# Performance work log

Hardware: AMD Instinct MI355X
Metric: run time of the kernel (lower is better)

The kernel has to match this reference:

```python
import jax, jax.numpy as jnp
import numpy as np

Q_SIZE, K_SIZE, H = 256, 256, 128
N, n, m, D_V = 4, 512, 512, 256

def setup_inputs() -> dict:
    key = jax.random.key(0)
    k1, k2, k3, k4, k5, k6 = jax.random.split(key, 6)
    return {
        "query": jax.random.normal(k1, (N, n, Q_SIZE), dtype=jnp.float32),
        "key": jax.random.normal(k2, (N, m, K_SIZE), dtype=jnp.float32),
        "value": jax.random.normal(k3, (N, m, D_V), dtype=jnp.float32),
        "W_q": jax.random.normal(k4, (Q_SIZE, H), dtype=jnp.float32) / np.sqrt(Q_SIZE),
        "W_k": jax.random.normal(k5, (K_SIZE, H), dtype=jnp.float32) / np.sqrt(K_SIZE),
        "W_v": jax.random.normal(k6, (H,), dtype=jnp.float32) / np.sqrt(H),
    }

def reference(query, key, value, W_q, W_k, W_v):
    q = query @ W_q                      # (N, n, h)
    k = key @ W_k                        # (N, m, h)
    # broadcast additive scores: tanh((N,n,1,h) + (N,1,m,h)) reduced by W_v -> (N,n,m)
    feats = jnp.tanh(q[:, :, None, :] + k[:, None, :, :])
    scores = jnp.einsum('bnmh,h->bnm', feats, W_v)
    attn = jax.nn.softmax(scores, axis=-1)  # softmax over keys m
    return jnp.einsum('bnm,bmd->bnd', attn, value)
```

## Files before the change

### kernel.cpp

```cpp
#include <hip/hip_runtime.h>
#include <math.h>

#define NB   4
#define SEQN 512
#define SEQM 512
#define QS   256
#define HH   128
#define DV   256
#define BM   (NB * SEQM)

static constexpr float kPreScale = 2.8853900817779268f;
static constexpr float kLog2e    = 1.4426950408889634f;

#if __has_builtin(__builtin_amdgcn_exp2f)
__device__ __forceinline__ float fexp2(float x) { return __builtin_amdgcn_exp2f(x); }
#else
__device__ __forceinline__ float fexp2(float x) { return exp2f(x); }
#endif

#if __has_builtin(__builtin_amdgcn_rcpf)
__device__ __forceinline__ float frcp(float x) { return __builtin_amdgcn_rcpf(x); }
#else
__device__ __forceinline__ float frcp(float x) { return 1.0f / x; }
#endif

__global__ __launch_bounds__(512) void proj_kernel(
    const float* __restrict__ query, const float* __restrict__ key,
    const float* __restrict__ Wq, const float* __restrict__ Wk,
    const float* __restrict__ wv,
    float* __restrict__ qt, float2* __restrict__ kt) {
  const int t = threadIdx.x;
  const int half = (NB * SEQN) / 8;
  const bool isK = blockIdx.x >= half;
  const int rb   = isK ? (blockIdx.x - half) : blockIdx.x;
  const float* __restrict__ in = isK ? key : query;
  const float* __restrict__ W  = isK ? Wk  : Wq;
  const int row0 = rb * 8;

  const int j  = t & 127;
  const int r0 = __builtin_amdgcn_readfirstlane((t >> 7) * 2);

  const float* __restrict__ x0p = in + (size_t)(row0 + r0 + 0) * QS;
  const float* __restrict__ x1p = in + (size_t)(row0 + r0 + 1) * QS;

  float a0 = 0.f, a1 = 0.f;
  for (int k0 = 0; k0 < QS; k0 += 4) {
    const float w0 = W[(k0 + 0) * HH + j];
    const float w1 = W[(k0 + 1) * HH + j];
    const float w2 = W[(k0 + 2) * HH + j];
    const float w3 = W[(k0 + 3) * HH + j];
    const float4 x0 = *reinterpret_cast<const float4*>(x0p + k0);
    const float4 x1 = *reinterpret_cast<const float4*>(x1p + k0);
    a0 = fmaf(x0.x, w0, fmaf(x0.y, w1, fmaf(x0.z, w2, fmaf(x0.w, w3, a0))));
    a1 = fmaf(x1.x, w0, fmaf(x1.y, w1, fmaf(x1.z, w2, fmaf(x1.w, w3, a1))));
  }
  const float wvj = wv[j];
  float acc[2] = {a0, a1};
#pragma unroll
  for (int r = 0; r < 2; ++r) {
    const float e  = fexp2(acc[r] * kPreScale);
    const float rc = frcp(e + 1.0f);
    float A = fmaf(-2.0f, rc, 1.0f);
    A = fminf(fmaxf(A, -0.99999988f), 0.99999988f);
    const int grow = row0 + r0 + r;
    if (isK) {
      kt[(size_t)j * BM + grow] = make_float2(A, wvj * A);
    } else {
      qt[(size_t)grow * (2 * HH) + j]      = A;
      qt[(size_t)grow * (2 * HH) + HH + j] = wvj * A;
    }
  }
}

__global__ __launch_bounds__(1024) void fused_kernel(
    const float* __restrict__ qt, const float2* __restrict__ kt,
    const float* __restrict__ value, float* __restrict__ out) {
  __shared__ float sp[8][SEQM];
  __shared__ float pvbuf[4][8][DV];
  __shared__ float rsh[8];

  const int t  = threadIdx.x;
  const int b  = blockIdx.x >> 6;
  const int n0 = (blockIdx.x & 63) * 8;
  const int m  = t & 511;
  const int nq4 = __builtin_amdgcn_readfirstlane((t >> 9) * 4);

  const float* __restrict__ qb = qt + ((size_t)b * SEQN + n0 + nq4) * (2 * HH);
  const float2* __restrict__ kb = kt + (size_t)b * SEQM + m;

  float N[4], D[4];
#pragma unroll
  for (int n = 0; n < 4; ++n) { N[n] = 0.f; D[n] = 1.f; }

  float2 fb[8];
#pragma unroll
  for (int jj = 0; jj < 8; ++jj) fb[jj] = kb[(size_t)jj * BM];

  for (int h0 = 0; h0 < HH; h0 += 8) {
    float kA[8], kW[8];
#pragma unroll
    for (int jj = 0; jj < 8; ++jj) { kA[jj] = fb[jj].x; kW[jj] = fb[jj].y; }
    if (h0 + 8 < HH) {
#pragma unroll
      for (int jj = 0; jj < 8; ++jj) fb[jj] = kb[(size_t)(h0 + 8 + jj) * BM];
    }
#pragma unroll
    for (int n = 0; n < 4; ++n) {
      const float* qr = qb + n * (2 * HH);
      const float4 a0 = *reinterpret_cast<const float4*>(qr + h0);
      const float4 a1 = *reinterpret_cast<const float4*>(qr + h0 + 4);
      const float4 v0 = *reinterpret_cast<const float4*>(qr + HH + h0);
      const float4 v1 = *reinterpret_cast<const float4*>(qr + HH + h0 + 4);
      const float s0 = v0.x + kW[0], d0 = fmaf(a0.x, kA[0], 1.0f);
      const float s1 = v0.y + kW[1], d1 = fmaf(a0.y, kA[1], 1.0f);
      const float s2 = v0.z + kW[2], d2 = fmaf(a0.z, kA[2], 1.0f);
      const float s3 = v0.w + kW[3], d3 = fmaf(a0.w, kA[3], 1.0f);
      const float s4 = v1.x + kW[4], d4 = fmaf(a1.x, kA[4], 1.0f);
      const float s5 = v1.y + kW[5], d5 = fmaf(a1.y, kA[5], 1.0f);
      const float s6 = v1.z + kW[6], d6 = fmaf(a1.z, kA[6], 1.0f);
      const float s7 = v1.w + kW[7], d7 = fmaf(a1.w, kA[7], 1.0f);
      const float t01 = fmaf(s0, d1, s1 * d0), e01 = d0 * d1;
      const float t23 = fmaf(s2, d3, s3 * d2), e23 = d2 * d3;
      const float t45 = fmaf(s4, d5, s5 * d4), e45 = d4 * d5;
      const float t67 = fmaf(s6, d7, s7 * d6), e67 = d6 * d7;
      const float t03 = fmaf(t01, e23, t23 * e01), e03 = e01 * e23;
      const float t47 = fmaf(t45, e67, t67 * e45), e47 = e45 * e67;
      const float t07 = fmaf(t03, e47, t47 * e03), e07 = e03 * e47;
      N[n] = fmaf(N[n], e07, t07 * D[n]);
      D[n] *= e07;
    }
  }
#pragma unroll
  for (int n = 0; n < 4; ++n) sp[nq4 + n][m] = N[n] * frcp(D[n]);
  __syncthreads();

  const int wave = t >> 6;
  const int lane = t & 63;
  const int row  = wave >> 1;
  const int hf   = wave & 1;
  float v[8];
  float mx = -1e30f;
#pragma unroll
  for (int i = 0; i < 8; ++i) {
    v[i] = sp[row][lane + 64 * i];
    mx = fmaxf(mx, v[i]);
  }
#pragma unroll
  for (int off = 32; off > 0; off >>= 1) mx = fmaxf(mx, __shfl_xor(mx, off));
  float p[8];
  float sum = 0.f;
#pragma unroll
  for (int i = 0; i < 8; ++i) {
    p[i] = fexp2((v[i] - mx) * kLog2e);
    sum += p[i];
  }
#pragma unroll
  for (int off = 32; off > 0; off >>= 1) sum += __shfl_xor(sum, off);
  __syncthreads();
#pragma unroll
  for (int i = 4 * hf; i < 4 * hf + 4; ++i) sp[row][lane + 64 * i] = p[i];
  if (hf == 0 && lane == 0) rsh[row] = frcp(sum);
  __syncthreads();

  const float* __restrict__ vb = value + (size_t)b * SEQM * DV;
  const int dp = (t & 127) * 2;
  const int mg = t >> 7;
  float o[8][2];
#pragma unroll
  for (int n = 0; n < 8; ++n) { o[n][0] = 0.f; o[n][1] = 0.f; }
  const int mbeg = mg * 64;
  for (int mi = 0; mi < 64; mi += 4) {
    const int m0 = mbeg + mi;
    const float2 w0 = *reinterpret_cast<const float2*>(vb + (size_t)(m0 + 0) * DV + dp);
    const float2 w1 = *reinterpret_cast<const float2*>(vb + (size_t)(m0 + 1) * DV + dp);
    const float2 w2 = *reinterpret_cast<const float2*>(vb + (size_t)(m0 + 2) * DV + dp);
    const float2 w3 = *reinterpret_cast<const float2*>(vb + (size_t)(m0 + 3) * DV + dp);
#pragma unroll
    for (int n = 0; n < 8; ++n) {
      const float4 p4 = *reinterpret_cast<const float4*>(&sp[n][m0]);
      o[n][0] = fmaf(p4.x, w0.x, fmaf(p4.y, w1.x, fmaf(p4.z, w2.x, fmaf(p4.w, w3.x, o[n][0]))));
      o[n][1] = fmaf(p4.x, w0.y, fmaf(p4.y, w1.y, fmaf(p4.z, w2.y, fmaf(p4.w, w3.y, o[n][1]))));
    }
  }
  if (mg >= 4) {
#pragma unroll
    for (int n = 0; n < 8; ++n)
      *reinterpret_cast<float2*>(&pvbuf[mg - 4][n][dp]) = make_float2(o[n][0], o[n][1]);
  }
  __syncthreads();
  if (mg < 4) {
#pragma unroll
    for (int n = 0; n < 8; ++n) {
      float2 prev = *reinterpret_cast<const float2*>(&pvbuf[mg][n][dp]);
      prev.x += o[n][0]; prev.y += o[n][1];
      *reinterpret_cast<float2*>(&pvbuf[mg][n][dp]) = prev;
    }
  }
  __syncthreads();

  {
    const int n = t >> 7;
    const int d = t & 127;
    const float rsn = rsh[n];
    float accA = 0.f, accB = 0.f;
#pragma unroll
    for (int g = 0; g < 4; ++g) {
      accA += pvbuf[g][n][d];
      accB += pvbuf[g][n][d + 128];
    }
    const size_t ob = ((size_t)b * SEQN + n0 + n) * DV;
    out[ob + d]       = accA * rsn;
    out[ob + d + 128] = accB * rsn;
  }
}

extern "C" void kernel_launch(void* const* d_in, const int* in_sizes, int n_in,
                              void* d_out, int out_size, void* d_ws, size_t ws_size,
                              hipStream_t stream) {
  const float* query = (const float*)d_in[0];
  const float* key   = (const float*)d_in[1];
  const float* value = (const float*)d_in[2];
  const float* W_q   = (const float*)d_in[3];
  const float* W_k   = (const float*)d_in[4];
  const float* W_v   = (const float*)d_in[5];
  float* out = (float*)d_out;

  float*  qt = (float*)d_out;
  float2* kt = (float2*)d_ws;

  proj_kernel<<<2 * (NB * SEQN) / 8, 512, 0, stream>>>(query, key, W_q, W_k, W_v, qt, kt);
  fused_kernel<<<NB * (SEQN / 8), 1024, 0, stream>>>(qt, kt, value, out);
}
```

Before: 48.03 us.

## Store only tanh(k) and tile score loop as 2 queries by 2 keys

The key projection buffer now holds only tanh(k) instead of the (A, wv*A) pair. The fused kernel recomputes wv*A per key from W_v loaded in registers. Each thread now computes a 2x2 block (2 query rows by 2 adjacent keys) rather than 4 query rows for 1 key, so each qt load is reused across two keys. This halves the workspace traffic for the key side, at the cost of extra multiplies to rebuild wv*A and different register pressure.

```diff
diff --git a/kernel.cpp b/kernel.cpp
--- a/kernel.cpp
+++ b/kernel.cpp
@@ -28,7 +28,7 @@
     const float* __restrict__ query, const float* __restrict__ key,
     const float* __restrict__ Wq, const float* __restrict__ Wk,
     const float* __restrict__ wv,
-    float* __restrict__ qt, float2* __restrict__ kt) {
+    float* __restrict__ qt, float* __restrict__ ktA) {
   const int t = threadIdx.x;
   const int half = (NB * SEQN) / 8;
   const bool isK = blockIdx.x >= half;
@@ -64,7 +64,7 @@
     A = fminf(fmaxf(A, -0.99999988f), 0.99999988f);
     const int grow = row0 + r0 + r;
     if (isK) {
-      kt[(size_t)j * BM + grow] = make_float2(A, wvj * A);
+      ktA[(size_t)j * BM + grow] = A;
     } else {
       qt[(size_t)grow * (2 * HH) + j]      = A;
       qt[(size_t)grow * (2 * HH) + HH + j] = wvj * A;
@@ -73,8 +73,9 @@
 }
 
 __global__ __launch_bounds__(1024) void fused_kernel(
-    const float* __restrict__ qt, const float2* __restrict__ kt,
-    const float* __restrict__ value, float* __restrict__ out) {
+    const float* __restrict__ qt, const float* __restrict__ ktA,
+    const float* __restrict__ wv, const float* __restrict__ value,
+    float* __restrict__ out) {
   __shared__ float sp[8][SEQM];
   __shared__ float pvbuf[4][8][DV];
   __shared__ float rsh[8];
@@ -82,56 +83,77 @@
   const int t  = threadIdx.x;
   const int b  = blockIdx.x >> 6;
   const int n0 = (blockIdx.x & 63) * 8;
-  const int m  = t & 511;
-  const int nq4 = __builtin_amdgcn_readfirstlane((t >> 9) * 4);
-
-  const float* __restrict__ qb = qt + ((size_t)b * SEQN + n0 + nq4) * (2 * HH);
-  const float2* __restrict__ kb = kt + (size_t)b * SEQM + m;
-
-  float N[4], D[4];
-#pragma unroll
-  for (int n = 0; n < 4; ++n) { N[n] = 0.f; D[n] = 1.f; }
+  const int mslot = t & 255;
+  const int m0 = 2 * mslot;
+  const int g2 = __builtin_amdgcn_readfirstlane((t >> 8) * 2);
+
+  const float* __restrict__ qb = qt + ((size_t)b * SEQN + n0 + g2) * (2 * HH);
+  const float* __restrict__ kb = ktA + (size_t)b * SEQM + m0;
+
+  float N00 = 0.f, N01 = 0.f, N10 = 0.f, N11 = 0.f;
+  float D00 = 1.f, D01 = 1.f, D10 = 1.f, D11 = 1.f;
 
   float2 fb[8];
 #pragma unroll
-  for (int jj = 0; jj < 8; ++jj) fb[jj] = kb[(size_t)jj * BM];
+  for (int jj = 0; jj < 8; ++jj) fb[jj] = *reinterpret_cast<const float2*>(kb + (size_t)jj * BM);
 
   for (int h0 = 0; h0 < HH; h0 += 8) {
-    float kA[8], kW[8];
-#pragma unroll
-    for (int jj = 0; jj < 8; ++jj) { kA[jj] = fb[jj].x; kW[jj] = fb[jj].y; }
+    float bA0[8], bA1[8];
+#pragma unroll
+    for (int jj = 0; jj < 8; ++jj) { bA0[jj] = fb[jj].x; bA1[jj] = fb[jj].y; }
     if (h0 + 8 < HH) {
 #pragma unroll
-      for (int jj = 0; jj < 8; ++jj) fb[jj] = kb[(size_t)(h0 + 8 + jj) * BM];
-    }
-#pragma unroll
-    for (int n = 0; n < 4; ++n) {
+      for (int jj = 0; jj < 8; ++jj)
+        fb[jj] = *reinterpret_cast<const float2*>(kb + (size_t)(h0 + 8 + jj) * BM);
+    }
+    const float4 wva = *reinterpret_cast<const float4*>(wv + h0);
+    const float4 wvb = *reinterpret_cast<const float4*>(wv + h0 + 4);
+    float u0[8], u1[8];
+    u0[0] = wva.x * bA0[0]; u1[0] = wva.x * bA1[0];
+    u0[1] = wva.y * bA0[1]; u1[1] = wva.y * bA1[1];
+    u0[2] = wva.z * bA0[2]; u1[2] = wva.z * bA1[2];
+    u0[3] = wva.w * bA0[3]; u1[3] = wva.w * bA1[3];
+    u0[4] = wvb.x * bA0[4]; u1[4] = wvb.x * bA1[4];
+    u0[5] = wvb.y * bA0[5]; u1[5] = wvb.y * bA1[5];
+    u0[6] = wvb.z * bA0[6]; u1[6] = wvb.z * bA1[6];
+    u0[7] = wvb.w * bA0[7]; u1[7] = wvb.w * bA1[7];
+#pragma unroll
+    for (int n = 0; n < 2; ++n) {
       const float* qr = qb + n * (2 * HH);
       const float4 a0 = *reinterpret_cast<const float4*>(qr + h0);
       const float4 a1 = *reinterpret_cast<const float4*>(qr + h0 + 4);
       const float4 v0 = *reinterpret_cast<const float4*>(qr + HH + h0);
       const float4 v1 = *reinterpret_cast<const float4*>(qr + HH + h0 + 4);
-      const float s0 = v0.x + kW[0], d0 = fmaf(a0.x, kA[0], 1.0f);
-      const float s1 = v0.y + kW[1], d1 = fmaf(a0.y, kA[1], 1.0f);
-      const float s2 = v0.z + kW[2], d2 = fmaf(a0.z, kA[2], 1.0f);
-      const float s3 = v0.w + kW[3], d3 = fmaf(a0.w, kA[3], 1.0f);
-      const float s4 = v1.x + kW[4], d4 = fmaf(a1.x, kA[4], 1.0f);
-      const float s5 = v1.y + kW[5], d5 = fmaf(a1.y, kA[5], 1.0f);
-      const float s6 = v1.z + kW[6], d6 = fmaf(a1.z, kA[6], 1.0f);
-      const float s7 = v1.w + kW[7], d7 = fmaf(a1.w, kA[7], 1.0f);
-      const float t01 = fmaf(s0, d1, s1 * d0), e01 = d0 * d1;
-      const float t23 = fmaf(s2, d3, s3 * d2), e23 = d2 * d3;
-      const float t45 = fmaf(s4, d5, s5 * d4), e45 = d4 * d5;
-      const float t67 = fmaf(s6, d7, s7 * d6), e67 = d6 * d7;
-      const float t03 = fmaf(t01, e23, t23 * e01), e03 = e01 * e23;
-      const float t47 = fmaf(t45, e67, t67 * e45), e47 = e45 * e67;
-      const float t07 = fmaf(t03, e47, t47 * e03), e07 = e03 * e47;
-      N[n] = fmaf(N[n], e07, t07 * D[n]);
-      D[n] *= e07;
-    }
-  }
-#pragma unroll
-  for (int n = 0; n < 4; ++n) sp[nq4 + n][m] = N[n] * frcp(D[n]);
+#pragma unroll
+      for (int mm = 0; mm < 2; ++mm) {
+        const float* bA = (mm == 0) ? bA0 : bA1;
+        const float* uu = (mm == 0) ? u0 : u1;
+        const float s0 = v0.x + uu[0], d0 = fmaf(a0.x, bA[0], 1.0f);
+        const float s1 = v0.y + uu[1], d1 = fmaf(a0.y, bA[1], 1.0f);
+        const float s2 = v0.z + uu[2], d2 = fmaf(a0.z, bA[2], 1.0f);
+        const float s3 = v0.w + uu[3], d3 = fmaf(a0.w, bA[3], 1.0f);
+        const float s4 = v1.x + uu[4], d4 = fmaf(a1.x, bA[4], 1.0f);
+        const float s5 = v1.y + uu[5], d5 = fmaf(a1.y, bA[5], 1.0f);
+        const float s6 = v1.z + uu[6], d6 = fmaf(a1.z, bA[6], 1.0f);
+        const float s7 = v1.w + uu[7], d7 = fmaf(a1.w, bA[7], 1.0f);
+        const float t01 = fmaf(s0, d1, s1 * d0), e01 = d0 * d1;
+        const float t23 = fmaf(s2, d3, s3 * d2), e23 = d2 * d3;
+        const float t45 = fmaf(s4, d5, s5 * d4), e45 = d4 * d5;
+        const float t67 = fmaf(s6, d7, s7 * d6), e67 = d6 * d7;
+        const float t03 = fmaf(t01, e23, t23 * e01), e03 = e01 * e23;
+        const float t47 = fmaf(t45, e67, t67 * e45), e47 = e45 * e67;
+        const float t07 = fmaf(t03, e47, t47 * e03), e07 = e03 * e47;
+        if (n == 0 && mm == 0) { N00 = fmaf(N00, e07, t07 * D00); D00 *= e07; }
+        if (n == 0 && mm == 1) { N01 = fmaf(N01, e07, t07 * D01); D01 *= e07; }
+        if (n == 1 && mm == 0) { N10 = fmaf(N10, e07, t07 * D10); D10 *= e07; }
+        if (n == 1 && mm == 1) { N11 = fmaf(N11, e07, t07 * D11); D11 *= e07; }
+      }
+    }
+  }
+  sp[g2 + 0][m0 + 0] = N00 * frcp(D00);
+  sp[g2 + 0][m0 + 1] = N01 * frcp(D01);
+  sp[g2 + 1][m0 + 0] = N10 * frcp(D10);
+  sp[g2 + 1][m0 + 1] = N11 * frcp(D11);
   __syncthreads();
 
   const int wave = t >> 6;
@@ -170,14 +192,14 @@
   for (int n = 0; n < 8; ++n) { o[n][0] = 0.f; o[n][1] = 0.f; }
   const int mbeg = mg * 64;
   for (int mi = 0; mi < 64; mi += 4) {
-    const int m0 = mbeg + mi;
-    const float2 w0 = *reinterpret_cast<const float2*>(vb + (size_t)(m0 + 0) * DV + dp);
-    const float2 w1 = *reinterpret_cast<const float2*>(vb + (size_t)(m0 + 1) * DV + dp);
-    const float2 w2 = *reinterpret_cast<const float2*>(vb + (size_t)(m0 + 2) * DV + dp);
-    const float2 w3 = *reinterpret_cast<const float2*>(vb + (size_t)(m0 + 3) * DV + dp);
+    const int mq = mbeg + mi;
+    const float2 w0 = *reinterpret_cast<const float2*>(vb + (size_t)(mq + 0) * DV + dp);
+    const float2 w1 = *reinterpret_cast<const float2*>(vb + (size_t)(mq + 1) * DV + dp);
+    const float2 w2 = *reinterpret_cast<const float2*>(vb + (size_t)(mq + 2) * DV + dp);
+    const float2 w3 = *reinterpret_cast<const float2*>(vb + (size_t)(mq + 3) * DV + dp);
 #pragma unroll
     for (int n = 0; n < 8; ++n) {
-      const float4 p4 = *reinterpret_cast<const float4*>(&sp[n][m0]);
+      const float4 p4 = *reinterpret_cast<const float4*>(&sp[n][mq]);
       o[n][0] = fmaf(p4.x, w0.x, fmaf(p4.y, w1.x, fmaf(p4.z, w2.x, fmaf(p4.w, w3.x, o[n][0]))));
       o[n][1] = fmaf(p4.x, w0.y, fmaf(p4.y, w1.y, fmaf(p4.z, w2.y, fmaf(p4.w, w3.y, o[n][1]))));
     }
@@ -225,9 +247,9 @@
   const float* W_v   = (const float*)d_in[5];
   float* out = (float*)d_out;
 
-  float*  qt = (float*)d_out;
-  float2* kt = (float2*)d_ws;
-
-  proj_kernel<<<2 * (NB * SEQN) / 8, 512, 0, stream>>>(query, key, W_q, W_k, W_v, qt, kt);
-  fused_kernel<<<NB * (SEQN / 8), 1024, 0, stream>>>(qt, kt, value, out);
+  float* qt  = (float*)d_out;
+  float* ktA = (float*)d_ws;
+
+  proj_kernel<<<2 * (NB * SEQN) / 8, 512, 0, stream>>>(query, key, W_q, W_k, W_v, qt, ktA);
+  fused_kernel<<<NB * (SEQN / 8), 1024, 0, stream>>>(qt, ktA, W_v, value, out);
 }
```

Measured after the change: 47.81 us. No clear change (-0.5%).
